# Performance work log

Measured on AMD Instinct MI355X. Metric: run time of the kernel, lower is better.

## Reference

```python
import jax, jax.numpy as jnp
import numpy as np

B, S, D = 4, 2048, 512
H = 8
DH = D // H
NEG = -9e15


def setup_inputs() -> dict:
    key = jax.random.key(0)
    ks = jax.random.split(key, 6)
    x = jax.random.normal(ks[0], (B, S, D), dtype=jnp.float32)
    mask = jax.random.randint(ks[1], (B, S), 0, 2, dtype=jnp.int32)
    # Linear params (torch convention: W [out, in], y = x @ W.T + b)
    lim_qkv = 1.0 / np.sqrt(D)
    W_qkv = jax.random.uniform(ks[2], (3 * D, D), jnp.float32, -lim_qkv, lim_qkv)
    b_qkv = jax.random.uniform(ks[3], (3 * D,), jnp.float32, -lim_qkv, lim_qkv)
    lim_o = 1.0 / np.sqrt(D)
    W_o = jax.random.uniform(ks[4], (D, D), jnp.float32, -lim_o, lim_o)
    b_o = jax.random.uniform(ks[5], (D,), jnp.float32, -lim_o, lim_o)
    return {"x": x, "mask": mask, "W_qkv": W_qkv, "b_qkv": b_qkv, "W_o": W_o, "b_o": b_o}


def reference(x, mask, W_qkv, b_qkv, W_o, b_o):
    b, s, d = x.shape
    # fused QKV projection: [B,S,3D]
    qkv = jnp.einsum('bsd,ed->bse', x, W_qkv) + b_qkv
    qkv = qkv.reshape(b, s, H, 3 * DH).transpose(0, 2, 1, 3)  # [B,H,S,3*DH]
    q, k, v = jnp.split(qkv, 3, axis=-1)  # each [B,H,S,DH]
    logits = jnp.einsum('bhqd,bhkd->bhqk', q, k) / jnp.sqrt(jnp.float32(DH))
    m = mask[:, None, None, :]  # [B,1,1,S]
    logits = jnp.where(m == 0, jnp.float32(NEG), logits)
    attn = jax.nn.softmax(logits, axis=-1)  # [B,H,S,S]
    values = jnp.einsum('bhqk,bhkd->bhqd', attn, v)
    values = values.transpose(0, 2, 1, 3).reshape(b, s, d)
    o = jnp.einsum('bsd,ed->bse', values, W_o) + b_o
    return o
```

## Files before the change

### kernel.cpp

```cpp
#include <hip/hip_runtime.h>
#include <stdint.h>

#define Bv 4
#define Sv 2048
#define Dv 512
#define Hv 8
#define E3 1536

typedef unsigned short u16;
typedef __bf16 bf16x8 __attribute__((ext_vector_type(8)));
typedef float f32x4 __attribute__((ext_vector_type(4)));

__device__ __forceinline__ u16 f2b(float f) {
  union { float f; uint32_t u; } v; v.f = f;
  uint32_t r = v.u + 0x7FFFu + ((v.u >> 16) & 1u);
  return (u16)(r >> 16);
}

__device__ __forceinline__ void gl_lds16(const void* g, void* l) {
  __builtin_amdgcn_global_load_lds(
      (__attribute__((address_space(1))) void*)(uintptr_t)g,
      (__attribute__((address_space(3))) void*)(uintptr_t)l, 16, 0, 0);
}

__global__ __launch_bounds__(256) void k_cast(const float* __restrict__ in,
                                              u16* __restrict__ out, int n8) {
  int i = blockIdx.x * 256 + threadIdx.x;
  if (i >= n8) return;
  const float4* p = (const float4*)in;
  float4 a = p[(size_t)i * 2], b = p[(size_t)i * 2 + 1];
  union { u16 h[8]; uint4 v; } r;
  r.h[0] = f2b(a.x); r.h[1] = f2b(a.y); r.h[2] = f2b(a.z); r.h[3] = f2b(a.w);
  r.h[4] = f2b(b.x); r.h[5] = f2b(b.y); r.h[6] = f2b(b.z); r.h[7] = f2b(b.w);
  ((uint4*)out)[i] = r.v;
}

template <int OUTF32>
__global__ __launch_bounds__(256) void k_gemm_bt(const u16* __restrict__ A,
                                                 const u16* __restrict__ Bw,
                                                 const float* __restrict__ bias,
                                                 void* __restrict__ C, int N, int K) {
  __shared__ alignas(16) u16 As[128][32];
  __shared__ alignas(16) u16 Bs[128][32];
  const int tid = threadIdx.x, lane = tid & 63, w = tid >> 6;
  const int quad = lane >> 4, l16 = lane & 15;
  const int wm = w & 1, wn = w >> 1;
  const size_t m0 = (size_t)blockIdx.y * 128;
  const int n0 = blockIdx.x * 128;
  const int srow = lane >> 2, scol = (lane & 3) * 8;
  f32x4 acc[4][4] = {};
  for (int k0 = 0; k0 < K; k0 += 32) {
    #pragma unroll
    for (int c = 0; c < 2; ++c) {
      const int rb = (w * 2 + c) * 16;
      gl_lds16(A + (m0 + rb + srow) * K + k0 + scol, &As[rb][0]);
      gl_lds16(Bw + (size_t)(n0 + rb + srow) * K + k0 + scol, &Bs[rb][0]);
    }
    __syncthreads();
    bf16x8 af[4], bfr[4];
    #pragma unroll
    for (int t = 0; t < 4; ++t) {
      af[t]  = *(const bf16x8*)&As[wm * 64 + t * 16 + l16][quad * 8];
      bfr[t] = *(const bf16x8*)&Bs[wn * 64 + t * 16 + l16][quad * 8];
    }
    #pragma unroll
    for (int mt = 0; mt < 4; ++mt)
      #pragma unroll
      for (int nt = 0; nt < 4; ++nt)
        acc[mt][nt] = __builtin_amdgcn_mfma_f32_16x16x32_bf16(af[mt], bfr[nt],
                                                              acc[mt][nt], 0, 0, 0);
    __syncthreads();
  }
  #pragma unroll
  for (int nt = 0; nt < 4; ++nt) {
    const int col = n0 + wn * 64 + nt * 16 + l16;
    const float bv = bias[col];
    #pragma unroll
    for (int mt = 0; mt < 4; ++mt) {
      const size_t row = m0 + wm * 64 + mt * 16 + quad * 4;
      #pragma unroll
      for (int r = 0; r < 4; ++r) {
        float v = acc[mt][nt][r] + bv;
        if (OUTF32) ((float*)C)[(row + r) * N + col] = v;
        else        ((u16*)C)[(row + r) * N + col] = f2b(v);
      }
    }
  }
}

__global__ __launch_bounds__(256) void k_pack(const u16* __restrict__ qkv,
                                              const int* __restrict__ mask,
                                              u16* __restrict__ kp,
                                              u16* __restrict__ vp,
                                              float* __restrict__ mbias) {
  __shared__ alignas(16) u16 T[64][72];
  const int tid = threadIdx.x;
  const int bh = blockIdx.y, b = bh >> 3, h = bh & 7;
  const int s0 = blockIdx.x * 64;
  if (h == 0 && tid < 64) {
    const int s = b * Sv + s0 + tid;
    mbias[s] = mask[s] ? 0.0f : -1e30f;
  }
  const size_t kpb = (size_t)bh * 128 * 1024;
  for (int idx = tid; idx < 512; idx += 256) {
    int r = idx >> 3, c8 = idx & 7;
    uint4 d = *(const uint4*)(qkv + (size_t)(b * Sv + s0 + r) * E3 + h * 192 + 64 + c8 * 8);
    int tile = (s0 >> 4) + (r >> 4), half = c8 >> 2, quad = c8 & 3, l16 = r & 15;
    *(uint4*)(kp + kpb + (size_t)tile * 1024 + half * 512 + (quad * 16 + l16) * 8) = d;
  }
  for (int idx = tid; idx < 512; idx += 256) {
    int r = idx >> 3, c = idx & 7;
    *(uint4*)&T[r][c * 8] =
        *(const uint4*)(qkv + ((size_t)(b * Sv + s0 + r)) * E3 + h * 192 + 128 + c * 8);
  }
  __syncthreads();
  const size_t vpb = (size_t)bh * 64 * 2048;
  for (int idx = tid; idx < 512; idx += 256) {
    int cc = idx >> 8, rest = idx & 255, dh = rest >> 2, kq = rest & 3;
    union { u16 h[8]; uint4 v; } rr;
    #pragma unroll
    for (int j = 0; j < 8; ++j) rr.h[j] = T[cc * 32 + kq * 8 + j][dh];
    int chunk = (s0 >> 5) + cc, nt2 = dh >> 4;
    *(uint4*)(vp + vpb + ((size_t)(chunk * 4 + nt2)) * 512 + (kq * 16 + (dh & 15)) * 8) = rr.v;
  }
}

__global__ __launch_bounds__(256) void k_attn(const u16* __restrict__ qkv,
                                              const u16* __restrict__ kp,
                                              const u16* __restrict__ vp,
                                              const float* __restrict__ mbias,
                                              u16* __restrict__ vals) {
  __shared__ alignas(16) u16 Ps[4][16][136];
  const int tid = threadIdx.x, lane = tid & 63, w = tid >> 6;
  const int quad = lane >> 4, l16 = lane & 15;
  const int bh = blockIdx.y, b = bh >> 3, h = bh & 7;
  const int q0 = blockIdx.x * 64 + w * 16;

  const u16* qrow = qkv + (size_t)(b * Sv + q0 + l16) * E3 + h * 192 + quad * 8;
  bf16x8 aq0 = *(const bf16x8*)qrow;
  bf16x8 aq1 = *(const bf16x8*)(qrow + 32);

  bf16x8 bones;
  {
    union { u16 u; __bf16 b; } one; one.u = 0x3F80;
    #pragma unroll
    for (int j = 0; j < 8; ++j) bones[j] = one.b;
  }

  f32x4 La = {0.f, 0.f, 0.f, 0.f};
  f32x4 Oa[4] = {};

  const u16* kpb = kp + (size_t)bh * 128 * 1024 + lane * 8;
  const u16* vpb = vp + (size_t)bh * 64 * 2048 + lane * 8;
  const float* mrow = mbias + b * Sv + l16;
  u16* ps_w = &Ps[w][0][0];
  const float cs = 0.18033688011112042f;

  #pragma unroll 1
  for (int k0 = 0; k0 < Sv; k0 += 128) {
    const int t0 = k0 >> 4, c0 = k0 >> 5;
    f32x4 Sa[8] = {};
    #pragma unroll
    for (int nt = 0; nt < 8; ++nt) {
      const u16* tb = kpb + (size_t)(t0 + nt) * 1024;
      bf16x8 bk0 = *(const bf16x8*)tb;
      bf16x8 bk1 = *(const bf16x8*)(tb + 512);
      Sa[nt] = __builtin_amdgcn_mfma_f32_16x16x32_bf16(aq0, bk0, Sa[nt], 0, 0, 0);
      Sa[nt] = __builtin_amdgcn_mfma_f32_16x16x32_bf16(aq1, bk1, Sa[nt], 0, 0, 0);
    }
    #pragma unroll
    for (int nt = 0; nt < 8; ++nt) {
      const float mb = mrow[k0 + nt * 16];
      #pragma unroll
      for (int r = 0; r < 4; ++r) {
        union { float f; uint32_t u; } pv;
        pv.f = __builtin_amdgcn_exp2f(fmaf(Sa[nt][r], cs, mb));
        ps_w[(quad * 4 + r) * 136 + nt * 16 + l16] = (u16)(pv.u >> 16);
      }
    }
    #pragma unroll
    for (int ks = 0; ks < 4; ++ks) {
      bf16x8 ap = *(const bf16x8*)(ps_w + l16 * 136 + ks * 32 + quad * 8);
      La = __builtin_amdgcn_mfma_f32_16x16x32_bf16(ap, bones, La, 0, 0, 0);
      #pragma unroll
      for (int nt2 = 0; nt2 < 4; ++nt2) {
        bf16x8 bv8 = *(const bf16x8*)(vpb + (size_t)((c0 + ks) * 4 + nt2) * 512);
        Oa[nt2] = __builtin_amdgcn_mfma_f32_16x16x32_bf16(ap, bv8, Oa[nt2], 0, 0, 0);
      }
    }
  }

  float li[4];
  #pragma unroll
  for (int r = 0; r < 4; ++r) li[r] = 1.0f / La[r];
  #pragma unroll
  for (int nt2 = 0; nt2 < 4; ++nt2)
    #pragma unroll
    for (int r = 0; r < 4; ++r) {
      const size_t srow = (size_t)(b * Sv + q0 + quad * 4 + r);
      vals[srow * Dv + h * 64 + nt2 * 16 + l16] = f2b(Oa[nt2][r] * li[r]);
    }
}

extern "C" void kernel_launch(void* const* d_in, const int* in_sizes, int n_in,
                              void* d_out, int out_size, void* d_ws, size_t ws_size,
                              hipStream_t stream) {
  const float* x    = (const float*)d_in[0];
  const int*   mask = (const int*)d_in[1];
  const float* Wqkv = (const float*)d_in[2];
  const float* bqkv = (const float*)d_in[3];
  const float* Wo   = (const float*)d_in[4];
  const float* bo   = (const float*)d_in[5];
  float* out = (float*)d_out;

  char* ws = (char*)d_ws;
  u16* xb    = (u16*)(ws + 0);
  u16* wqkvb = (u16*)(ws + 8388608);
  u16* wob   = (u16*)(ws + 9961472);
  u16* qkv   = (u16*)(ws + 10485760);
  u16* kp    = (u16*)(ws + 35651584);
  u16* vals  = (u16*)(ws + 44040192);
  u16* vp    = (u16*)(ws + 0);
  float* mbias = (float*)(ws + 8388608);

  k_cast<<<2048, 256, 0, stream>>>(x, xb, 524288);
  k_cast<<<384, 256, 0, stream>>>(Wqkv, wqkvb, 98304);
  k_cast<<<128, 256, 0, stream>>>(Wo, wob, 32768);
  k_gemm_bt<0><<<dim3(12, 64), 256, 0, stream>>>(xb, wqkvb, bqkv, qkv, E3, Dv);
  k_pack<<<dim3(32, 32), 256, 0, stream>>>(qkv, mask, kp, vp, mbias);
  k_attn<<<dim3(32, 32), 256, 0, stream>>>(qkv, kp, vp, mbias, vals);
  k_gemm_bt<1><<<dim3(4, 64), 256, 0, stream>>>(vals, wob, bo, out, Dv, Dv);
}
```

Measured before the change: 218.1 us.

## Split attention key range across wave pairs and merge casts into one launch

Each attention block now covers 32 query rows instead of 64. Two waves share the same 16 rows, and each processes half of the key sequence. Their partial outputs and row sums are combined through LDS after a barrier, which doubles the grid and shortens each wave's serial loop. The change also pads the P tile pitch to cut LDS bank conflicts, adds a launch-bounds occupancy hint, and merges the three cast kernels into one launch. In exchange it adds a block-wide sync, a reduction through LDS, and duplicate Q loads per block.

New measurement: 286.8 us. 31.5% more time.

```diff
diff --git a/kernel.cpp b/kernel.cpp
--- a/kernel.cpp
+++ b/kernel.cpp
@@ -6,6 +6,7 @@
 #define Dv 512
 #define Hv 8
 #define E3 1536
+#define PPITCH 164
 
 typedef unsigned short u16;
 typedef __bf16 bf16x8 __attribute__((ext_vector_type(8)));
@@ -23,10 +24,17 @@
       (__attribute__((address_space(3))) void*)(uintptr_t)l, 16, 0, 0);
 }
 
-__global__ __launch_bounds__(256) void k_cast(const float* __restrict__ in,
-                                              u16* __restrict__ out, int n8) {
-  int i = blockIdx.x * 256 + threadIdx.x;
-  if (i >= n8) return;
+__global__ __launch_bounds__(256) void k_cast3(const float* __restrict__ x,
+                                               const float* __restrict__ wqkv,
+                                               const float* __restrict__ wo,
+                                               u16* __restrict__ xb,
+                                               u16* __restrict__ wqkvb,
+                                               u16* __restrict__ wob) {
+  const int bid = blockIdx.x;
+  const float* in; u16* out; int i;
+  if (bid < 2048)      { in = x;    out = xb;    i = bid * 256 + threadIdx.x; }
+  else if (bid < 2432) { in = wqkv; out = wqkvb; i = (bid - 2048) * 256 + threadIdx.x; }
+  else                 { in = wo;   out = wob;   i = (bid - 2432) * 256 + threadIdx.x; }
   const float4* p = (const float4*)in;
   float4 a = p[(size_t)i * 2], b = p[(size_t)i * 2 + 1];
   union { u16 h[8]; uint4 v; } r;
@@ -125,16 +133,18 @@
   }
 }
 
-__global__ __launch_bounds__(256) void k_attn(const u16* __restrict__ qkv,
-                                              const u16* __restrict__ kp,
-                                              const u16* __restrict__ vp,
-                                              const float* __restrict__ mbias,
-                                              u16* __restrict__ vals) {
-  __shared__ alignas(16) u16 Ps[4][16][136];
+__global__ __launch_bounds__(256, 7) void k_attn(const u16* __restrict__ qkv,
+                                                 const u16* __restrict__ kp,
+                                                 const u16* __restrict__ vp,
+                                                 const float* __restrict__ mbias,
+                                                 u16* __restrict__ vals) {
+  __shared__ alignas(16) u16 Ps[4][16 * PPITCH];
   const int tid = threadIdx.x, lane = tid & 63, w = tid >> 6;
   const int quad = lane >> 4, l16 = lane & 15;
   const int bh = blockIdx.y, b = bh >> 3, h = bh & 7;
-  const int q0 = blockIdx.x * 64 + w * 16;
+  const int sidx = (blockIdx.x << 1) | (w & 1);
+  const int half = w >> 1;
+  const int q0 = sidx * 16;
 
   const u16* qrow = qkv + (size_t)(b * Sv + q0 + l16) * E3 + h * 192 + quad * 8;
   bf16x8 aq0 = *(const bf16x8*)qrow;
@@ -153,11 +163,12 @@
   const u16* kpb = kp + (size_t)bh * 128 * 1024 + lane * 8;
   const u16* vpb = vp + (size_t)bh * 64 * 2048 + lane * 8;
   const float* mrow = mbias + b * Sv + l16;
-  u16* ps_w = &Ps[w][0][0];
+  u16* ps_w = &Ps[w][0];
   const float cs = 0.18033688011112042f;
+  const int k_begin = half * (Sv / 2), k_end = k_begin + Sv / 2;
 
   #pragma unroll 1
-  for (int k0 = 0; k0 < Sv; k0 += 128) {
+  for (int k0 = k_begin; k0 < k_end; k0 += 128) {
     const int t0 = k0 >> 4, c0 = k0 >> 5;
     f32x4 Sa[8] = {};
     #pragma unroll
@@ -175,12 +186,12 @@
       for (int r = 0; r < 4; ++r) {
         union { float f; uint32_t u; } pv;
         pv.f = __builtin_amdgcn_exp2f(fmaf(Sa[nt][r], cs, mb));
-        ps_w[(quad * 4 + r) * 136 + nt * 16 + l16] = (u16)(pv.u >> 16);
+        ps_w[(quad * 4 + r) * PPITCH + nt * 16 + l16] = (u16)(pv.u >> 16);
       }
     }
     #pragma unroll
     for (int ks = 0; ks < 4; ++ks) {
-      bf16x8 ap = *(const bf16x8*)(ps_w + l16 * 136 + ks * 32 + quad * 8);
+      bf16x8 ap = *(const bf16x8*)(ps_w + l16 * PPITCH + ks * 32 + quad * 8);
       La = __builtin_amdgcn_mfma_f32_16x16x32_bf16(ap, bones, La, 0, 0, 0);
       #pragma unroll
       for (int nt2 = 0; nt2 < 4; ++nt2) {
@@ -190,16 +201,27 @@
     }
   }
 
-  float li[4];
-  #pragma unroll
-  for (int r = 0; r < 4; ++r) li[r] = 1.0f / La[r];
-  #pragma unroll
-  for (int nt2 = 0; nt2 < 4; ++nt2)
-    #pragma unroll
-    for (int r = 0; r < 4; ++r) {
-      const size_t srow = (size_t)(b * Sv + q0 + quad * 4 + r);
-      vals[srow * Dv + h * 64 + nt2 * 16 + l16] = f2b(Oa[nt2][r] * li[r]);
-    }
+  if (half == 1) {
+    f32x4* fl = (f32x4*)((float*)&Ps[w][0] + lane * 20);
+    fl[0] = Oa[0]; fl[1] = Oa[1]; fl[2] = Oa[2]; fl[3] = Oa[3]; fl[4] = La;
+  }
+  __syncthreads();
+  if (half == 0) {
+    const f32x4* fl = (const f32x4*)((const float*)&Ps[w + 2][0] + lane * 20);
+    #pragma unroll
+    for (int i = 0; i < 4; ++i) Oa[i] += fl[i];
+    La += fl[4];
+    float li[4];
+    #pragma unroll
+    for (int r = 0; r < 4; ++r) li[r] = 1.0f / La[r];
+    #pragma unroll
+    for (int nt2 = 0; nt2 < 4; ++nt2)
+      #pragma unroll
+      for (int r = 0; r < 4; ++r) {
+        const size_t srow = (size_t)(b * Sv + q0 + quad * 4 + r);
+        vals[srow * Dv + h * 64 + nt2 * 16 + l16] = f2b(Oa[nt2][r] * li[r]);
+      }
+  }
 }
 
 extern "C" void kernel_launch(void* const* d_in, const int* in_sizes, int n_in,
@@ -223,11 +245,9 @@
   u16* vp    = (u16*)(ws + 0);
   float* mbias = (float*)(ws + 8388608);
 
-  k_cast<<<2048, 256, 0, stream>>>(x, xb, 524288);
-  k_cast<<<384, 256, 0, stream>>>(Wqkv, wqkvb, 98304);
-  k_cast<<<128, 256, 0, stream>>>(Wo, wob, 32768);
+  k_cast3<<<2560, 256, 0, stream>>>(x, Wqkv, Wo, xb, wqkvb, wob);
   k_gemm_bt<0><<<dim3(12, 64), 256, 0, stream>>>(xb, wqkvb, bqkv, qkv, E3, Dv);
   k_pack<<<dim3(32, 32), 256, 0, stream>>>(qkv, mask, kp, vp, mbias);
-  k_attn<<<dim3(32, 32), 256, 0, stream>>>(qkv, kp, vp, mbias, vals);
+  k_attn<<<dim3(64, 32), 256, 0, stream>>>(qkv, kp, vp, mbias, vals);
   k_gemm_bt<1><<<dim3(4, 64), 256, 0, stream>>>(vals, wob, bo, out, Dv, Dv);
 }
```
